# Performance work log

Hardware: AMD Instinct MI355X
Metric: run time of the kernel (lower is better)

## Reference

```python
import jax, jax.numpy as jnp
import numpy as np

EPS = 1e-5

def _layernorm(x, w, b):
    mu = jnp.mean(x, axis=-1, keepdims=True)
    var = jnp.mean(jnp.square(x - mu), axis=-1, keepdims=True)
    return (x - mu) * jax.lax.rsqrt(var + EPS) * w + b

def setup_inputs() -> dict:
    key = jax.random.key(0)
    ks = jax.random.split(key, 16)
    B, N, CZ, C = 1, 384, 128, 128
    s_z = 1.0 / np.sqrt(CZ)
    s_c = 1.0 / np.sqrt(C)
    inp = {
        "pair": jax.random.normal(ks[0], (B, N, N, CZ), jnp.float32),
        "ln_pair_w": jnp.ones((CZ,), jnp.float32),
        "ln_pair_b": jnp.zeros((CZ,), jnp.float32),
        "ln_out_w": jnp.ones((C,), jnp.float32),
        "ln_out_b": jnp.zeros((C,), jnp.float32),
        "g1_w": jax.random.uniform(ks[1], (C, CZ), jnp.float32, -s_z, s_z),
        "g1_b": jax.random.uniform(ks[2], (C,), jnp.float32, -s_z, s_z),
        "g2_w": jax.random.uniform(ks[3], (C, CZ), jnp.float32, -s_z, s_z),
        "g2_b": jax.random.uniform(ks[4], (C,), jnp.float32, -s_z, s_z),
        "l1_w": jax.random.uniform(ks[5], (C, CZ), jnp.float32, -s_z, s_z),
        "l1_b": jax.random.uniform(ks[6], (C,), jnp.float32, -s_z, s_z),
        "l2_w": jax.random.uniform(ks[7], (C, CZ), jnp.float32, -s_z, s_z),
        "l2_b": jax.random.uniform(ks[8], (C,), jnp.float32, -s_z, s_z),
        "gate_w": jax.random.uniform(ks[9], (CZ, CZ), jnp.float32, -s_z, s_z),
        "gate_b": jax.random.uniform(ks[10], (CZ,), jnp.float32, -s_z, s_z),
        "out_w": jax.random.uniform(ks[11], (CZ, C), jnp.float32, -s_c, s_c),
        "out_b": jax.random.uniform(ks[12], (CZ,), jnp.float32, -s_c, s_c),
    }
    return inp

def reference(pair, ln_pair_w, ln_pair_b, ln_out_w, ln_out_b,
              g1_w, g1_b, g2_w, g2_b, l1_w, l1_b, l2_w, l2_b,
              gate_w, gate_b, out_w, out_b):
    z = _layernorm(pair, ln_pair_w, ln_pair_b)                    # [B,N,N,cz]
    A = jax.nn.sigmoid(z @ g1_w.T + g1_b) * (z @ l1_w.T + l1_b)  # [B,N,N,c]
    Bm = jax.nn.sigmoid(z @ g2_w.T + g2_b) * (z @ l2_w.T + l2_b) # [B,N,N,c]
    G = jax.nn.sigmoid(z @ gate_w.T + gate_b)                     # [B,N,N,cz]
    vals = jnp.einsum('bikc,bjkc->bijc', A, Bm)                   # [B,N,N,c]
    out = G * (_layernorm(vals, ln_out_w, ln_out_b) @ out_w.T + out_b)
    return out
```

## Files before the change

kernel.cpp:

```cpp
#include <hip/hip_runtime.h>
#include <hip/hip_fp16.h>

#define NDIM 384
#define NN   147456
#define CZC  128

typedef _Float16 f16x8 __attribute__((ext_vector_type(8)));
typedef float    f32x4 __attribute__((ext_vector_type(4)));

static __device__ __forceinline__ unsigned short f2h(float f) {
  return __builtin_bit_cast(unsigned short, __float2half(f));
}
static __device__ __forceinline__ float h2f(unsigned short s) {
  return __half2float(__builtin_bit_cast(__half, s));
}
static __device__ __forceinline__ unsigned pk2(float lo, float hi) {
  return (unsigned)f2h(lo) | ((unsigned)f2h(hi) << 16);
}
static __device__ __forceinline__ float sigmoidf_(float x) {
  return __builtin_amdgcn_rcpf(1.0f + __expf(-x));
}

__global__ void k0_conv(const float* __restrict__ g1, const float* __restrict__ l1,
                        const float* __restrict__ g2, const float* __restrict__ l2,
                        const float* __restrict__ gw, const float* __restrict__ ow,
                        unsigned short* __restrict__ Wh)
{
  const int m = blockIdx.x >> 6;
  const float* s = (m == 0) ? g1 : (m == 1) ? l1 : (m == 2) ? g2 : (m == 3) ? l2
                 : (m == 4) ? gw : ow;
  const int e = (blockIdx.x & 63) * 256 + threadIdx.x;
  Wh[m * 16384 + e] = f2h(s[e]);
}

__global__ __launch_bounds__(512, 4) void k1_proj(
    const float* __restrict__ pair, const float* __restrict__ lnw, const float* __restrict__ lnb,
    const unsigned short* __restrict__ Wh,
    const float* __restrict__ g1b, const float* __restrict__ l1b,
    const float* __restrict__ g2b, const float* __restrict__ l2b,
    const float* __restrict__ gtb,
    unsigned short* __restrict__ Ah, unsigned short* __restrict__ Bh,
    unsigned short* __restrict__ G)
{
  __shared__ char zb[32768];
  __shared__ char sb[32768];
  const int t   = threadIdx.x;
  const int xcd = blockIdx.x & 7;
  const int r0  = (xcd * 144 + (blockIdx.x >> 3)) * 128;

  {
    const int rl = t >> 2, quad = t & 3, c0 = quad * 32;
    const float4* src = reinterpret_cast<const float4*>(pair + (size_t)(r0 + rl) * CZC + c0);
    float v[32];
    float s = 0.f, ss = 0.f;
#pragma unroll
    for (int q = 0; q < 8; ++q) {
      float4 f4 = src[q];
      v[4*q] = f4.x; v[4*q+1] = f4.y; v[4*q+2] = f4.z; v[4*q+3] = f4.w;
    }
#pragma unroll
    for (int j = 0; j < 32; ++j) { s += v[j]; ss += v[j] * v[j]; }
    s  += __shfl_xor(s, 1);  s  += __shfl_xor(s, 2);
    ss += __shfl_xor(ss, 1); ss += __shfl_xor(ss, 2);
    const float mu   = s * (1.f / 128.f);
    const float rstd = rsqrtf(ss * (1.f / 128.f) - mu * mu + 1e-5f);
    unsigned u[16];
#pragma unroll
    for (int q = 0; q < 8; ++q) {
      float4 w4 = reinterpret_cast<const float4*>(lnw + c0)[q];
      float4 b4 = reinterpret_cast<const float4*>(lnb + c0)[q];
      float z0 = (v[4*q  ] - mu) * rstd * w4.x + b4.x;
      float z1 = (v[4*q+1] - mu) * rstd * w4.y + b4.y;
      float z2 = (v[4*q+2] - mu) * rstd * w4.z + b4.z;
      float z3 = (v[4*q+3] - mu) * rstd * w4.w + b4.w;
      u[2*q] = pk2(z0, z1); u[2*q+1] = pk2(z2, z3);
    }
#pragma unroll
    for (int g = 0; g < 4; ++g) {
      int gi = quad * 4 + g;
      *reinterpret_cast<uint4*>(zb + rl * 256 + 16 * (gi ^ (rl & 7))) =
          make_uint4(u[4*g], u[4*g+1], u[4*g+2], u[4*g+3]);
    }
  }
  __syncthreads();

  const int w = t >> 6, l = t & 63;
  const int lrow = l & 15, lk = l >> 4;
  const int col = w * 16 + lrow;

  auto ldA = [&](int h, int mt, int ks) -> f16x8 {
    int row = h * 64 + mt * 16 + lrow;
    int gi  = ks * 4 + lk;
    return *reinterpret_cast<const f16x8*>(zb + row * 256 + 16 * (gi ^ (row & 7)));
  };
  auto ldB = [&](const unsigned short* Wm, int ks) -> f16x8 {
    return *reinterpret_cast<const f16x8*>(Wm + col * 128 + ks * 32 + lk * 8);
  };
  auto stageh = [&](int h, int mt, unsigned lo, unsigned hi) {
    int gran = h * 8 + mt * 2 + (lk >> 1);
    *reinterpret_cast<uint2*>(sb + col * 256 + 16 * (gran ^ (col & 15)) + (lk & 1) * 8)
        = make_uint2(lo, hi);
  };
  auto flush = [&](unsigned short* Ot) {
#pragma unroll
    for (int q = 0; q < 4; ++q) {
      int i = t + 512 * q;
      int cl = i >> 4, sl = i & 15;
      uint4 u = *reinterpret_cast<const uint4*>(sb + cl * 256 + 16 * (sl ^ (cl & 15)));
      *reinterpret_cast<uint4*>(Ot + (size_t)cl * NN + r0 + sl * 8) = u;
    }
  };

  auto do_pair = [&](const unsigned short* Wg, const unsigned short* Wl,
                     const float* bgp, const float* blp, unsigned short* Ot) {
    __syncthreads();
    const float gb = bgp[col], lb = blp[col];
#pragma unroll
    for (int h = 0; h < 2; ++h) {
      f32x4 accg[4], accl[4];
#pragma unroll
      for (int mt = 0; mt < 4; ++mt) { accg[mt] = 0.f; accl[mt] = 0.f; }
#pragma unroll
      for (int ks = 0; ks < 4; ++ks) {
        f16x8 af[4];
#pragma unroll
        for (int mt = 0; mt < 4; ++mt) af[mt] = ldA(h, mt, ks);
        f16x8 bg_ = ldB(Wg, ks);
#pragma unroll
        for (int mt = 0; mt < 4; ++mt)
          accg[mt] = __builtin_amdgcn_mfma_f32_16x16x32_f16(af[mt], bg_, accg[mt], 0, 0, 0);
        f16x8 bl_ = ldB(Wl, ks);
#pragma unroll
        for (int mt = 0; mt < 4; ++mt)
          accl[mt] = __builtin_amdgcn_mfma_f32_16x16x32_f16(af[mt], bl_, accl[mt], 0, 0, 0);
      }
#pragma unroll
      for (int mt = 0; mt < 4; ++mt) {
        float a0 = sigmoidf_(accg[mt][0] + gb) * (accl[mt][0] + lb);
        float a1 = sigmoidf_(accg[mt][1] + gb) * (accl[mt][1] + lb);
        float a2 = sigmoidf_(accg[mt][2] + gb) * (accl[mt][2] + lb);
        float a3 = sigmoidf_(accg[mt][3] + gb) * (accl[mt][3] + lb);
        stageh(h, mt, pk2(a0, a1), pk2(a2, a3));
      }
    }
    __syncthreads();
    flush(Ot);
  };

  do_pair(Wh + 0 * 16384, Wh + 1 * 16384, g1b, l1b, Ah);
  do_pair(Wh + 2 * 16384, Wh + 3 * 16384, g2b, l2b, Bh);

  if (G) {
    __syncthreads();
    const unsigned short* Wg = Wh + 4 * 16384;
    const float gb = gtb[col];
#pragma unroll
    for (int h = 0; h < 2; ++h) {
      f32x4 acc[4];
#pragma unroll
      for (int mt = 0; mt < 4; ++mt) acc[mt] = 0.f;
#pragma unroll
      for (int ks = 0; ks < 4; ++ks) {
        f16x8 af[4];
#pragma unroll
        for (int mt = 0; mt < 4; ++mt) af[mt] = ldA(h, mt, ks);
        f16x8 bf_ = ldB(Wg, ks);
#pragma unroll
        for (int mt = 0; mt < 4; ++mt)
          acc[mt] = __builtin_amdgcn_mfma_f32_16x16x32_f16(af[mt], bf_, acc[mt], 0, 0, 0);
      }
#pragma unroll
      for (int mt = 0; mt < 4; ++mt)
        stageh(h, mt, pk2(sigmoidf_(acc[mt][0] + gb), sigmoidf_(acc[mt][1] + gb)),
                      pk2(sigmoidf_(acc[mt][2] + gb), sigmoidf_(acc[mt][3] + gb)));
    }
    __syncthreads();
    flush(G);
  }
}

__global__ __launch_bounds__(256) void k2_tri(
    const unsigned short* __restrict__ Ah, const unsigned short* __restrict__ Bh,
    unsigned short* __restrict__ v16)
{
  __shared__ char As[8192];
  __shared__ char Bs[8192];
  __shared__ char Vs[32768];
  const int x  = blockIdx.x & 7;
  const int r  = blockIdx.x >> 3;
  const int tt = r % 9;
  const int c  = (r / 9) * 8 + x;
  const int ib = (tt / 3) * 128, jb = (tt % 3) * 128;
  const size_t co = (size_t)c * NN;
  const int t = threadIdx.x, w = t >> 6, l = t & 63;
  const int wi = (w >> 1) * 64, wj = (w & 1) * 64;
  const int lrow = l & 15, lk = l >> 4;
  const int srow = t >> 2, sgr = t & 3;

  f32x4 acc[4][4];
#pragma unroll
  for (int mt = 0; mt < 4; ++mt)
#pragma unroll
    for (int nt = 0; nt < 4; ++nt) acc[mt][nt] = 0.f;

  for (int kb = 0; kb < 12; ++kb) {
    const size_t ka  = co + (size_t)(ib + srow) * NDIM + kb * 32 + sgr * 8;
    const size_t kb_ = co + (size_t)(jb + srow) * NDIM + kb * 32 + sgr * 8;
    uint4 a0 = *reinterpret_cast<const uint4*>(Ah + ka);
    uint4 a1 = *reinterpret_cast<const uint4*>(Ah + ka + 64 * NDIM);
    uint4 b0 = *reinterpret_cast<const uint4*>(Bh + kb_);
    uint4 b1 = *reinterpret_cast<const uint4*>(Bh + kb_ + 64 * NDIM);
    __syncthreads();
    const int g0 = 16 * (sgr ^ (srow & 3));
    *reinterpret_cast<uint4*>(As + srow * 64 + g0)        = a0;
    *reinterpret_cast<uint4*>(As + (srow + 64) * 64 + g0) = a1;
    *reinterpret_cast<uint4*>(Bs + srow * 64 + g0)        = b0;
    *reinterpret_cast<uint4*>(Bs + (srow + 64) * 64 + g0) = b1;
    __syncthreads();
    f16x8 af[4], bfr[4];
#pragma unroll
    for (int mt = 0; mt < 4; ++mt) {
      int row = wi + mt * 16 + lrow;
      af[mt] = *reinterpret_cast<const f16x8*>(As + row * 64 + 16 * (lk ^ (row & 3)));
    }
#pragma unroll
    for (int nt = 0; nt < 4; ++nt) {
      int row = wj + nt * 16 + lrow;
      bfr[nt] = *reinterpret_cast<const f16x8*>(Bs + row * 64 + 16 * (lk ^ (row & 3)));
    }
#pragma unroll
    for (int mt = 0; mt < 4; ++mt)
#pragma unroll
      for (int nt = 0; nt < 4; ++nt)
        acc[mt][nt] = __builtin_amdgcn_mfma_f32_16x16x32_f16(af[mt], bfr[nt], acc[mt][nt], 0, 0, 0);
  }

  __syncthreads();
#pragma unroll
  for (int mt = 0; mt < 4; ++mt)
#pragma unroll
    for (int nt = 0; nt < 4; ++nt) {
      const int j = wj + nt * 16 + lrow;
#pragma unroll
      for (int reg = 0; reg < 4; ++reg) {
        const int i = wi + mt * 16 + lk * 4 + reg;
        int sl = (j >> 3) ^ (i & 15);
        *reinterpret_cast<unsigned short*>(Vs + i * 256 + sl * 16 + (j & 7) * 2)
            = f2h(acc[mt][nt][reg]);
      }
    }
  __syncthreads();
  unsigned short* vc = v16 + co;
#pragma unroll
  for (int q = 0; q < 8; ++q) {
    int idx = t + 256 * q;
    int i = idx >> 4, sl = idx & 15;
    uint4 u = *reinterpret_cast<const uint4*>(Vs + i * 256 + ((sl ^ (i & 15)) * 16));
    *reinterpret_cast<uint4*>(vc + (size_t)(ib + i) * NDIM + jb + sl * 8) = u;
  }
}

__global__ __launch_bounds__(256, 4) void k3g(
    const unsigned short* __restrict__ v16, const unsigned short* __restrict__ G,
    const float* __restrict__ lnow, const float* __restrict__ lnob,
    const unsigned short* __restrict__ Wh, const float* __restrict__ outb,
    float* __restrict__ outp)
{
  __shared__ char smem[36864];
  unsigned short* vs = reinterpret_cast<unsigned short*>(smem);
  unsigned short* gs = reinterpret_cast<unsigned short*>(smem + 18432);
  char* zvb = smem;
  const int t  = threadIdx.x;
  const int p0 = blockIdx.x * 64;

#pragma unroll
  for (int q = 0; q < 4; ++q) {
    int ci = t + 256 * q;
    int c = ci >> 3, ch8 = ci & 7;
    uint4 u = *reinterpret_cast<const uint4*>(v16 + (size_t)c * NN + p0 + ch8 * 8);
    int g = ch8 ^ (c & 7);
    *reinterpret_cast<uint4*>(vs + c * 72 + g * 8) = u;
  }
#pragma unroll
  for (int q = 0; q < 4; ++q) {
    int ci = t + 256 * q;
    int c = ci >> 3, ch8 = ci & 7;
    uint4 u = *reinterpret_cast<const uint4*>(G + (size_t)c * NN + p0 + ch8 * 8);
    int g = ch8 ^ (c & 7);
    *reinterpret_cast<uint4*>(gs + c * 72 + g * 8) = u;
  }
  __syncthreads();

  const int w = t >> 6, l = t & 63;
  const int lrow = l & 15, lk = l >> 4;
  const int colbase = w * 32;

  {
    const int pl = t >> 2, quad = t & 3, c0q = quad * 32;
    float v[32];
#pragma unroll
    for (int j = 0; j < 32; ++j) {
      int c = c0q + j;
      v[j] = h2f(vs[c * 72 + (((pl >> 3) ^ (c & 7)) << 3) + (pl & 7)]);
    }
    float s = 0.f, ss = 0.f;
#pragma unroll
    for (int j = 0; j < 32; ++j) { s += v[j]; ss += v[j] * v[j]; }
    s  += __shfl_xor(s, 1);  s  += __shfl_xor(s, 2);
    ss += __shfl_xor(ss, 1); ss += __shfl_xor(ss, 2);
    const float mu   = s * (1.f / 128.f);
    const float rstd = rsqrtf(ss * (1.f / 128.f) - mu * mu + 1e-5f);
    unsigned u[16];
#pragma unroll
    for (int q = 0; q < 8; ++q) {
      float4 w4 = reinterpret_cast<const float4*>(lnow + c0q)[q];
      float4 b4 = reinterpret_cast<const float4*>(lnob + c0q)[q];
      float z0 = (v[4*q  ] - mu) * rstd * w4.x + b4.x;
      float z1 = (v[4*q+1] - mu) * rstd * w4.y + b4.y;
      float z2 = (v[4*q+2] - mu) * rstd * w4.z + b4.z;
      float z3 = (v[4*q+3] - mu) * rstd * w4.w + b4.w;
      u[2*q] = pk2(z0, z1); u[2*q+1] = pk2(z2, z3);
    }
    __syncthreads();
#pragma unroll
    for (int g = 0; g < 4; ++g) {
      int gi = quad * 4 + g;
      *reinterpret_cast<uint4*>(zvb + pl * 256 + 16 * (gi ^ (pl & 7))) =
          make_uint4(u[4*g], u[4*g+1], u[4*g+2], u[4*g+3]);
    }
  }
  __syncthreads();

  const unsigned short* Wo = Wh + 5 * 16384;
  f32x4 acc[4][2];
#pragma unroll
  for (int mt = 0; mt < 4; ++mt)
#pragma unroll
    for (int nt = 0; nt < 2; ++nt) acc[mt][nt] = 0.f;
#pragma unroll
  for (int ks = 0; ks < 4; ++ks) {
    f16x8 af[4];
#pragma unroll
    for (int mt = 0; mt < 4; ++mt) {
      int row = mt * 16 + lrow;
      int gi  = ks * 4 + lk;
      af[mt] = *reinterpret_cast<const f16x8*>(zvb + row * 256 + 16 * (gi ^ (row & 7)));
    }
#pragma unroll
    for (int nt = 0; nt < 2; ++nt) {
      int cz = colbase + nt * 16 + lrow;
      f16x8 bf_ = *reinterpret_cast<const f16x8*>(Wo + cz * 128 + ks * 32 + lk * 8);
#pragma unroll
      for (int mt = 0; mt < 4; ++mt)
        acc[mt][nt] = __builtin_amdgcn_mfma_f32_16x16x32_f16(af[mt], bf_, acc[mt][nt], 0, 0, 0);
    }
  }
#pragma unroll
  for (int mt = 0; mt < 4; ++mt)
#pragma unroll
    for (int nt = 0; nt < 2; ++nt) {
      int cz = colbase + nt * 16 + lrow;
      float ob = outb[cz];
#pragma unroll
      for (int reg = 0; reg < 4; ++reg) {
        int plc = mt * 16 + lk * 4 + reg;
        float gv = h2f(gs[cz * 72 + (((plc >> 3) ^ (cz & 7)) << 3) + (plc & 7)]);
        outp[(size_t)(p0 + plc) * CZC + cz] = gv * (acc[mt][nt][reg] + ob);
      }
    }
}

__global__ __launch_bounds__(256, 3) void k3r(
    const float* __restrict__ pair, const unsigned short* __restrict__ v16,
    const float* __restrict__ lnpw, const float* __restrict__ lnpb,
    const float* __restrict__ lnow, const float* __restrict__ lnob,
    const unsigned short* __restrict__ Wh,
    const float* __restrict__ gtb, const float* __restrict__ outb,
    float* __restrict__ outp)
{
  __shared__ char smem[53248];
  unsigned short* vs = reinterpret_cast<unsigned short*>(smem);
  char* zgb = smem + 18432;
  char* zvb = smem + 36864;
  const int t  = threadIdx.x;
  const int p0 = blockIdx.x * 64;

#pragma unroll
  for (int q = 0; q < 4; ++q) {
    int ci = t + 256 * q;
    int c = ci >> 3, ch8 = ci & 7;
    uint4 u = *reinterpret_cast<const uint4*>(v16 + (size_t)c * NN + p0 + ch8 * 8);
    int g = ch8 ^ (c & 7);
    *reinterpret_cast<uint4*>(vs + c * 72 + g * 8) = u;
  }
  {
    const int rl = t >> 2, quad = t & 3, c0 = quad * 32;
    const float4* src = reinterpret_cast<const float4*>(pair + (size_t)(p0 + rl) * CZC + c0);
    float v[32];
    float s = 0.f, ss = 0.f;
#pragma unroll
    for (int q = 0; q < 8; ++q) {
      float4 f4 = src[q];
      v[4*q] = f4.x; v[4*q+1] = f4.y; v[4*q+2] = f4.z; v[4*q+3] = f4.w;
    }
#pragma unroll
    for (int j = 0; j < 32; ++j) { s += v[j]; ss += v[j] * v[j]; }
    s  += __shfl_xor(s, 1);  s  += __shfl_xor(s, 2);
    ss += __shfl_xor(ss, 1); ss += __shfl_xor(ss, 2);
    const float mu   = s * (1.f / 128.f);
    const float rstd = rsqrtf(ss * (1.f / 128.f) - mu * mu + 1e-5f);
    unsigned u[16];
#pragma unroll
    for (int q = 0; q < 8; ++q) {
      float4 w4 = reinterpret_cast<const float4*>(lnpw + c0)[q];
      float4 b4 = reinterpret_cast<const float4*>(lnpb + c0)[q];
      float z0 = (v[4*q  ] - mu) * rstd * w4.x + b4.x;
      float z1 = (v[4*q+1] - mu) * rstd * w4.y + b4.y;
      float z2 = (v[4*q+2] - mu) * rstd * w4.z + b4.z;
      float z3 = (v[4*q+3] - mu) * rstd * w4.w + b4.w;
      u[2*q] = pk2(z0, z1); u[2*q+1] = pk2(z2, z3);
    }
#pragma unroll
    for (int g = 0; g < 4; ++g) {
      int gi = quad * 4 + g;
      *reinterpret_cast<uint4*>(zgb + rl * 256 + 16 * (gi ^ (rl & 7))) =
          make_uint4(u[4*g], u[4*g+1], u[4*g+2], u[4*g+3]);
    }
  }
  __syncthreads();

  const int w = t >> 6, l = t & 63;
  const int lrow = l & 15, lk = l >> 4;
  const int colbase = w * 32;

  auto ldZ = [&](const char* base, int mt, int ks) -> f16x8 {
    int row = mt * 16 + lrow;
    int gi  = ks * 4 + lk;
    return *reinterpret_cast<const f16x8*>(base + row * 256 + 16 * (gi ^ (row & 7)));
  };
  auto ldW = [&](const unsigned short* Wm, int nt, int ks) -> f16x8 {
    int cz = colbase + nt * 16 + lrow;
    return *reinterpret_cast<const f16x8*>(Wm + cz * 128 + ks * 32 + lk * 8);
  };

  f32x4 gacc[4][2];
#pragma unroll
  for (int mt = 0; mt < 4; ++mt)
#pragma unroll
    for (int nt = 0; nt < 2; ++nt) gacc[mt][nt] = 0.f;
  {
    const unsigned short* Wg = Wh + 4 * 16384;
#pragma unroll
    for (int ks = 0; ks < 4; ++ks) {
      f16x8 af[4];
#pragma unroll
      for (int mt = 0; mt < 4; ++mt) af[mt] = ldZ(zgb, mt, ks);
#pragma unroll
      for (int nt = 0; nt < 2; ++nt) {
        f16x8 bf_ = ldW(Wg, nt, ks);
#pragma unroll
        for (int mt = 0; mt < 4; ++mt)
          gacc[mt][nt] = __builtin_amdgcn_mfma_f32_16x16x32_f16(af[mt], bf_, gacc[mt][nt], 0, 0, 0);
      }
    }
  }

  {
    const int pl = t >> 2, quad = t & 3, c0q = quad * 32;
    float v[32];
#pragma unroll
    for (int j = 0; j < 32; ++j) {
      int c = c0q + j;
      v[j] = h2f(vs[c * 72 + (((pl >> 3) ^ (c & 7)) << 3) + (pl & 7)]);
    }
    float s = 0.f, ss = 0.f;
#pragma unroll
    for (int j = 0; j < 32; ++j) { s += v[j]; ss += v[j] * v[j]; }
    s  += __shfl_xor(s, 1);  s  += __shfl_xor(s, 2);
    ss += __shfl_xor(ss, 1); ss += __shfl_xor(ss, 2);
    const float mu   = s * (1.f / 128.f);
    const float rstd = rsqrtf(ss * (1.f / 128.f) - mu * mu + 1e-5f);
    unsigned u[16];
#pragma unroll
    for (int q = 0; q < 8; ++q) {
      float4 w4 = reinterpret_cast<const float4*>(lnow + c0q)[q];
      float4 b4 = reinterpret_cast<const float4*>(lnob + c0q)[q];
      float z0 = (v[4*q  ] - mu) * rstd * w4.x + b4.x;
      float z1 = (v[4*q+1] - mu) * rstd * w4.y + b4.y;
      float z2 = (v[4*q+2] - mu) * rstd * w4.z + b4.z;
      float z3 = (v[4*q+3] - mu) * rstd * w4.w + b4.w;
      u[2*q] = pk2(z0, z1); u[2*q+1] = pk2(z2, z3);
    }
#pragma unroll
    for (int g = 0; g < 4; ++g) {
      int gi = quad * 4 + g;
      *reinterpret_cast<uint4*>(zvb + pl * 256 + 16 * (gi ^ (pl & 7))) =
          make_uint4(u[4*g], u[4*g+1], u[4*g+2], u[4*g+3]);
    }
  }
  __syncthreads();

  const unsigned short* Wo = Wh + 5 * 16384;
  f32x4 acc[4][2];
#pragma unroll
  for (int mt = 0; mt < 4; ++mt)
#pragma unroll
    for (int nt = 0; nt < 2; ++nt) acc[mt][nt] = 0.f;
#pragma unroll
  for (int ks = 0; ks < 4; ++ks) {
    f16x8 af[4];
#pragma unroll
    for (int mt = 0; mt < 4; ++mt) af[mt] = ldZ(zvb, mt, ks);
#pragma unroll
    for (int nt = 0; nt < 2; ++nt) {
      f16x8 bf_ = ldW(Wo, nt, ks);
#pragma unroll
      for (int mt = 0; mt < 4; ++mt)
        acc[mt][nt] = __builtin_amdgcn_mfma_f32_16x16x32_f16(af[mt], bf_, acc[mt][nt], 0, 0, 0);
    }
  }
#pragma unroll
  for (int mt = 0; mt < 4; ++mt)
#pragma unroll
    for (int nt = 0; nt < 2; ++nt) {
      int cz = colbase + nt * 16 + lrow;
      float ob = outb[cz], gb = gtb[cz];
#pragma unroll
      for (int reg = 0; reg < 4; ++reg) {
        int plc = mt * 16 + lk * 4 + reg;
        float gv = sigmoidf_(gacc[mt][nt][reg] + gb);
        outp[(size_t)(p0 + plc) * CZC + cz] = gv * (acc[mt][nt][reg] + ob);
      }
    }
}

extern "C" void kernel_launch(void* const* d_in, const int* in_sizes, int n_in,
                              void* d_out, int out_size, void* d_ws, size_t ws_size,
                              hipStream_t stream)
{
  const float* pair      = (const float*)d_in[0];
  const float* ln_pair_w = (const float*)d_in[1];
  const float* ln_pair_b = (const float*)d_in[2];
  const float* ln_out_w  = (const float*)d_in[3];
  const float* ln_out_b  = (const float*)d_in[4];
  const float* g1_w      = (const float*)d_in[5];
  const float* g1_b      = (const float*)d_in[6];
  const float* g2_w      = (const float*)d_in[7];
  const float* g2_b      = (const float*)d_in[8];
  const float* l1_w      = (const float*)d_in[9];
  const float* l1_b      = (const float*)d_in[10];
  const float* l2_w      = (const float*)d_in[11];
  const float* l2_b      = (const float*)d_in[12];
  const float* gate_w    = (const float*)d_in[13];
  const float* gate_b    = (const float*)d_in[14];
  const float* out_w     = (const float*)d_in[15];
  const float* out_b     = (const float*)d_in[16];

  const size_t WH = 196608;
  const size_t H  = 37748736;
  char* ws  = (char*)d_ws;
  char* dob = (char*)d_out;

  unsigned short* Wp = (unsigned short*)ws;
  unsigned short* V  = (unsigned short*)(ws + WH);
  unsigned short* G  = (ws_size >= WH + 2 * H) ? (unsigned short*)(ws + WH + H) : nullptr;
  unsigned short* Ah = (unsigned short*)dob;
  unsigned short* Bh = (unsigned short*)(dob + H);

  k0_conv<<<384, 256, 0, stream>>>(g1_w, l1_w, g2_w, l2_w, gate_w, out_w, Wp);
  k1_proj<<<1152, 512, 0, stream>>>(pair, ln_pair_w, ln_pair_b, Wp,
                                    g1_b, l1_b, g2_b, l2_b, gate_b, Ah, Bh, G);
  k2_tri<<<1152, 256, 0, stream>>>(Ah, Bh, V);
  if (G)
    k3g<<<2304, 256, 0, stream>>>(V, G, ln_out_w, ln_out_b, Wp, out_b, (float*)d_out);
  else
    k3r<<<2304, 256, 0, stream>>>(pair, V, ln_pair_w, ln_pair_b, ln_out_w, ln_out_b,
                                  Wp, gate_b, out_b, (float*)d_out);
}
```

Measured before the change: 172.9 us.

## Halve k1_proj block size with each wave computing two column tiles

Shrinks the projection kernel's block from 512 to 256 threads. Each wave now covers 32 output columns (two 16-wide N tiles) instead of 16, so every A fragment loaded from shared memory feeds twice as many MFMAs. The LayerNorm prologue and the flush loop are reworked so each thread handles twice the rows and chunks. Register use roughly doubles for accumulators, which may lower occupancy, and the launch bounds change to 256 threads with at least 2 blocks per SIMD.

```diff
diff --git a/kernel.cpp b/kernel.cpp
--- a/kernel.cpp
+++ b/kernel.cpp
@@ -33,7 +33,7 @@
   Wh[m * 16384 + e] = f2h(s[e]);
 }
 
-__global__ __launch_bounds__(512, 4) void k1_proj(
+__global__ __launch_bounds__(256, 2) void k1_proj(
     const float* __restrict__ pair, const float* __restrict__ lnw, const float* __restrict__ lnb,
     const unsigned short* __restrict__ Wh,
     const float* __restrict__ g1b, const float* __restrict__ l1b,
@@ -50,61 +50,65 @@
 
   {
     const int rl = t >> 2, quad = t & 3, c0 = quad * 32;
-    const float4* src = reinterpret_cast<const float4*>(pair + (size_t)(r0 + rl) * CZC + c0);
-    float v[32];
-    float s = 0.f, ss = 0.f;
-#pragma unroll
-    for (int q = 0; q < 8; ++q) {
-      float4 f4 = src[q];
-      v[4*q] = f4.x; v[4*q+1] = f4.y; v[4*q+2] = f4.z; v[4*q+3] = f4.w;
-    }
-#pragma unroll
-    for (int j = 0; j < 32; ++j) { s += v[j]; ss += v[j] * v[j]; }
-    s  += __shfl_xor(s, 1);  s  += __shfl_xor(s, 2);
-    ss += __shfl_xor(ss, 1); ss += __shfl_xor(ss, 2);
-    const float mu   = s * (1.f / 128.f);
-    const float rstd = rsqrtf(ss * (1.f / 128.f) - mu * mu + 1e-5f);
-    unsigned u[16];
-#pragma unroll
-    for (int q = 0; q < 8; ++q) {
-      float4 w4 = reinterpret_cast<const float4*>(lnw + c0)[q];
-      float4 b4 = reinterpret_cast<const float4*>(lnb + c0)[q];
-      float z0 = (v[4*q  ] - mu) * rstd * w4.x + b4.x;
-      float z1 = (v[4*q+1] - mu) * rstd * w4.y + b4.y;
-      float z2 = (v[4*q+2] - mu) * rstd * w4.z + b4.z;
-      float z3 = (v[4*q+3] - mu) * rstd * w4.w + b4.w;
-      u[2*q] = pk2(z0, z1); u[2*q+1] = pk2(z2, z3);
-    }
-#pragma unroll
-    for (int g = 0; g < 4; ++g) {
-      int gi = quad * 4 + g;
-      *reinterpret_cast<uint4*>(zb + rl * 256 + 16 * (gi ^ (rl & 7))) =
-          make_uint4(u[4*g], u[4*g+1], u[4*g+2], u[4*g+3]);
+    for (int b = 0; b < 2; ++b) {
+      const int row = b * 64 + rl;
+      const float4* src = reinterpret_cast<const float4*>(pair + (size_t)(r0 + row) * CZC + c0);
+      float v[32];
+      float s = 0.f, ss = 0.f;
+#pragma unroll
+      for (int q = 0; q < 8; ++q) {
+        float4 f4 = src[q];
+        v[4*q] = f4.x; v[4*q+1] = f4.y; v[4*q+2] = f4.z; v[4*q+3] = f4.w;
+      }
+#pragma unroll
+      for (int j = 0; j < 32; ++j) { s += v[j]; ss += v[j] * v[j]; }
+      s  += __shfl_xor(s, 1);  s  += __shfl_xor(s, 2);
+      ss += __shfl_xor(ss, 1); ss += __shfl_xor(ss, 2);
+      const float mu   = s * (1.f / 128.f);
+      const float rstd = rsqrtf(ss * (1.f / 128.f) - mu * mu + 1e-5f);
+      unsigned u[16];
+#pragma unroll
+      for (int q = 0; q < 8; ++q) {
+        float4 w4 = reinterpret_cast<const float4*>(lnw + c0)[q];
+        float4 b4 = reinterpret_cast<const float4*>(lnb + c0)[q];
+        float z0 = (v[4*q  ] - mu) * rstd * w4.x + b4.x;
+        float z1 = (v[4*q+1] - mu) * rstd * w4.y + b4.y;
+        float z2 = (v[4*q+2] - mu) * rstd * w4.z + b4.z;
+        float z3 = (v[4*q+3] - mu) * rstd * w4.w + b4.w;
+        u[2*q] = pk2(z0, z1); u[2*q+1] = pk2(z2, z3);
+      }
+#pragma unroll
+      for (int g = 0; g < 4; ++g) {
+        int gi = quad * 4 + g;
+        *reinterpret_cast<uint4*>(zb + row * 256 + 16 * (gi ^ (row & 7))) =
+            make_uint4(u[4*g], u[4*g+1], u[4*g+2], u[4*g+3]);
+      }
     }
   }
   __syncthreads();
 
   const int w = t >> 6, l = t & 63;
   const int lrow = l & 15, lk = l >> 4;
-  const int col = w * 16 + lrow;
+  const int colbase = w * 32;
 
   auto ldA = [&](int h, int mt, int ks) -> f16x8 {
     int row = h * 64 + mt * 16 + lrow;
     int gi  = ks * 4 + lk;
     return *reinterpret_cast<const f16x8*>(zb + row * 256 + 16 * (gi ^ (row & 7)));
   };
-  auto ldB = [&](const unsigned short* Wm, int ks) -> f16x8 {
+  auto ldB = [&](const unsigned short* Wm, int nt, int ks) -> f16x8 {
+    int col = colbase + nt * 16 + lrow;
     return *reinterpret_cast<const f16x8*>(Wm + col * 128 + ks * 32 + lk * 8);
   };
-  auto stageh = [&](int h, int mt, unsigned lo, unsigned hi) {
+  auto stageh = [&](int col, int h, int mt, unsigned lo, unsigned hi) {
     int gran = h * 8 + mt * 2 + (lk >> 1);
     *reinterpret_cast<uint2*>(sb + col * 256 + 16 * (gran ^ (col & 15)) + (lk & 1) * 8)
         = make_uint2(lo, hi);
   };
   auto flush = [&](unsigned short* Ot) {
 #pragma unroll
-    for (int q = 0; q < 4; ++q) {
-      int i = t + 512 * q;
+    for (int q = 0; q < 8; ++q) {
+      int i = t + 256 * q;
       int cl = i >> 4, sl = i & 15;
       uint4 u = *reinterpret_cast<const uint4*>(sb + cl * 256 + 16 * (sl ^ (cl & 15)));
       *reinterpret_cast<uint4*>(Ot + (size_t)cl * NN + r0 + sl * 8) = u;
@@ -114,34 +118,42 @@
   auto do_pair = [&](const unsigned short* Wg, const unsigned short* Wl,
                      const float* bgp, const float* blp, unsigned short* Ot) {
     __syncthreads();
-    const float gb = bgp[col], lb = blp[col];
 #pragma unroll
     for (int h = 0; h < 2; ++h) {
-      f32x4 accg[4], accl[4];
-#pragma unroll
-      for (int mt = 0; mt < 4; ++mt) { accg[mt] = 0.f; accl[mt] = 0.f; }
+      f32x4 accg[4][2], accl[4][2];
+#pragma unroll
+      for (int mt = 0; mt < 4; ++mt)
+#pragma unroll
+        for (int nt = 0; nt < 2; ++nt) { accg[mt][nt] = 0.f; accl[mt][nt] = 0.f; }
 #pragma unroll
       for (int ks = 0; ks < 4; ++ks) {
         f16x8 af[4];
 #pragma unroll
         for (int mt = 0; mt < 4; ++mt) af[mt] = ldA(h, mt, ks);
-        f16x8 bg_ = ldB(Wg, ks);
-#pragma unroll
-        for (int mt = 0; mt < 4; ++mt)
-          accg[mt] = __builtin_amdgcn_mfma_f32_16x16x32_f16(af[mt], bg_, accg[mt], 0, 0, 0);
-        f16x8 bl_ = ldB(Wl, ks);
-#pragma unroll
-        for (int mt = 0; mt < 4; ++mt)
-          accl[mt] = __builtin_amdgcn_mfma_f32_16x16x32_f16(af[mt], bl_, accl[mt], 0, 0, 0);
-      }
-#pragma unroll
-      for (int mt = 0; mt < 4; ++mt) {
-        float a0 = sigmoidf_(accg[mt][0] + gb) * (accl[mt][0] + lb);
-        float a1 = sigmoidf_(accg[mt][1] + gb) * (accl[mt][1] + lb);
-        float a2 = sigmoidf_(accg[mt][2] + gb) * (accl[mt][2] + lb);
-        float a3 = sigmoidf_(accg[mt][3] + gb) * (accl[mt][3] + lb);
-        stageh(h, mt, pk2(a0, a1), pk2(a2, a3));
-      }
+#pragma unroll
+        for (int nt = 0; nt < 2; ++nt) {
+          f16x8 bg_ = ldB(Wg, nt, ks);
+#pragma unroll
+          for (int mt = 0; mt < 4; ++mt)
+            accg[mt][nt] = __builtin_amdgcn_mfma_f32_16x16x32_f16(af[mt], bg_, accg[mt][nt], 0, 0, 0);
+          f16x8 bl_ = ldB(Wl, nt, ks);
+#pragma unroll
+          for (int mt = 0; mt < 4; ++mt)
+            accl[mt][nt] = __builtin_amdgcn_mfma_f32_16x16x32_f16(af[mt], bl_, accl[mt][nt], 0, 0, 0);
+        }
+      }
+#pragma unroll
+      for (int mt = 0; mt < 4; ++mt)
+#pragma unroll
+        for (int nt = 0; nt < 2; ++nt) {
+          int col = colbase + nt * 16 + lrow;
+          float gb = bgp[col], lb = blp[col];
+          float a0 = sigmoidf_(accg[mt][nt][0] + gb) * (accl[mt][nt][0] + lb);
+          float a1 = sigmoidf_(accg[mt][nt][1] + gb) * (accl[mt][nt][1] + lb);
+          float a2 = sigmoidf_(accg[mt][nt][2] + gb) * (accl[mt][nt][2] + lb);
+          float a3 = sigmoidf_(accg[mt][nt][3] + gb) * (accl[mt][nt][3] + lb);
+          stageh(col, h, mt, pk2(a0, a1), pk2(a2, a3));
+        }
     }
     __syncthreads();
     flush(Ot);
@@ -153,26 +165,36 @@
   if (G) {
     __syncthreads();
     const unsigned short* Wg = Wh + 4 * 16384;
-    const float gb = gtb[col];
 #pragma unroll
     for (int h = 0; h < 2; ++h) {
-      f32x4 acc[4];
-#pragma unroll
-      for (int mt = 0; mt < 4; ++mt) acc[mt] = 0.f;
+      f32x4 acc[4][2];
+#pragma unroll
+      for (int mt = 0; mt < 4; ++mt)
+#pragma unroll
+        for (int nt = 0; nt < 2; ++nt) acc[mt][nt] = 0.f;
 #pragma unroll
       for (int ks = 0; ks < 4; ++ks) {
         f16x8 af[4];
 #pragma unroll
         for (int mt = 0; mt < 4; ++mt) af[mt] = ldA(h, mt, ks);
-        f16x8 bf_ = ldB(Wg, ks);
-#pragma unroll
-        for (int mt = 0; mt < 4; ++mt)
-          acc[mt] = __builtin_amdgcn_mfma_f32_16x16x32_f16(af[mt], bf_, acc[mt], 0, 0, 0);
+#pragma unroll
+        for (int nt = 0; nt < 2; ++nt) {
+          f16x8 bf_ = ldB(Wg, nt, ks);
+#pragma unroll
+          for (int mt = 0; mt < 4; ++mt)
+            acc[mt][nt] = __builtin_amdgcn_mfma_f32_16x16x32_f16(af[mt], bf_, acc[mt][nt], 0, 0, 0);
+        }
       }
 #pragma unroll
       for (int mt = 0; mt < 4; ++mt)
-        stageh(h, mt, pk2(sigmoidf_(acc[mt][0] + gb), sigmoidf_(acc[mt][1] + gb)),
-                      pk2(sigmoidf_(acc[mt][2] + gb), sigmoidf_(acc[mt][3] + gb)));
+#pragma unroll
+        for (int nt = 0; nt < 2; ++nt) {
+          int col = colbase + nt * 16 + lrow;
+          float gb = gtb[col];
+          stageh(col, h, mt,
+                 pk2(sigmoidf_(acc[mt][nt][0] + gb), sigmoidf_(acc[mt][nt][1] + gb)),
+                 pk2(sigmoidf_(acc[mt][nt][2] + gb), sigmoidf_(acc[mt][nt][3] + gb)));
+        }
     }
     __syncthreads();
     flush(G);
@@ -568,7 +590,7 @@
   unsigned short* Bh = (unsigned short*)(dob + H);
 
   k0_conv<<<384, 256, 0, stream>>>(g1_w, l1_w, g2_w, l2_w, gate_w, out_w, Wp);
-  k1_proj<<<1152, 512, 0, stream>>>(pair, ln_pair_w, ln_pair_b, Wp,
+  k1_proj<<<1152, 256, 0, stream>>>(pair, ln_pair_w, ln_pair_b, Wp,
                                     g1_b, l1_b, g2_b, l2_b, gate_b, Ah, Bh, G);
   k2_tri<<<1152, 256, 0, stream>>>(Ah, Bh, V);
   if (G)
```

After: 153.9 us. -11.0%, faster.
